# Kernel optimization log

Measured on AMD Instinct MI355X. Metric: run time of the kernel, lower is better.

## Reference

```python
import jax, jax.numpy as jnp
import numpy as np

N_NODES = 50000
N_EDGES = 800000
IN_C, HID_C, OUT_C = 128, 128, 40


def gcn_conv(x, W, b, src, dst, dinv):
    # x: [N, Fin] -> [N, Fout]; PyG GCNConv: h = W x, then sym-normalized
    # aggregation over edges (incl. self-loops), plus bias.
    h = x @ W  # [N, Fout]
    norm = dinv[src] * dinv[dst]  # [E+N]
    msg = h[src] * norm[:, None]  # gather + scale, [E+N, Fout]
    out = jax.ops.segment_sum(msg, dst, num_segments=x.shape[0])
    return out + b


def _prep_edges(edge_index, n):
    # add self-loops; compute deg^{-1/2} with unit edge weights
    loop = jnp.arange(n, dtype=edge_index.dtype)
    src = jnp.concatenate([edge_index[0], loop])
    dst = jnp.concatenate([edge_index[1], loop])
    deg = jax.ops.segment_sum(jnp.ones_like(dst, dtype=jnp.float32), dst, num_segments=n)
    dinv = jnp.where(deg > 0, jax.lax.rsqrt(jnp.maximum(deg, 1.0)), 0.0)
    return src, dst, dinv


def setup_inputs() -> dict:
    key = jax.random.key(0)
    ks = jax.random.split(key, 5)
    x = jax.random.normal(ks[0], (N_NODES, IN_C), dtype=jnp.float32)
    edge_index = jax.random.randint(ks[1], (2, N_EDGES), 0, N_NODES, dtype=jnp.int32)
    s = 0.05
    W1 = jax.random.normal(ks[2], (IN_C, HID_C), dtype=jnp.float32) * s
    W2 = jax.random.normal(ks[3], (HID_C, HID_C), dtype=jnp.float32) * s
    W3 = jax.random.normal(ks[4], (HID_C, OUT_C), dtype=jnp.float32) * s
    return {
        "x": x, "edge_index": edge_index,
        "W1": W1, "b1": jnp.zeros((HID_C,), jnp.float32),
        "W2": W2, "b2": jnp.zeros((HID_C,), jnp.float32),
        "W3": W3, "b3": jnp.zeros((OUT_C,), jnp.float32),
    }


def reference(x, edge_index, W1, b1, W2, b2, W3, b3):
    n = x.shape[0]
    src, dst, dinv = _prep_edges(edge_index, n)
    h = jax.nn.relu(gcn_conv(x, W1, b1, src, dst, dinv))  # dropout = id (eval)
    h = jax.nn.relu(gcn_conv(h, W2, b2, src, dst, dinv))
    h = gcn_conv(h, W3, b3, src, dst, dinv)
    return jax.nn.log_softmax(h, axis=1)
```

## Files before the change

kernel.cpp:

```cpp
#include <hip/hip_runtime.h>
#include <cmath>

__device__ __forceinline__ unsigned short f2bf(float f) {
  unsigned u = __float_as_uint(f);
  u = (u + 0x7FFFu + ((u >> 16) & 1u)) >> 16;
  return (unsigned short)u;
}
__device__ __forceinline__ unsigned pack2(float a, float b) {
  return (unsigned)f2bf(a) | ((unsigned)f2bf(b) << 16);
}
__device__ __forceinline__ float bflo(unsigned u) { return __uint_as_float(u << 16); }
__device__ __forceinline__ float bfhi(unsigned u) { return __uint_as_float(u & 0xFFFF0000u); }
__device__ __forceinline__ float bf1(unsigned short h) { return __uint_as_float((unsigned)h << 16); }

__device__ __forceinline__ unsigned char fp8e(float v) {
  unsigned u = __float_as_uint(v * 0x1.0p-120f);
  unsigned s = (u >> 24) & 0x80u;
  u &= 0x7FFFFFFFu;
  u = u + 0x000FFFFFu + ((u >> 20) & 1u);
  return (unsigned char)(s | ((u >> 20) & 0x7Fu));
}
__device__ __forceinline__ float fp8d(unsigned b) {
  unsigned u = ((b & 0x80u) << 24) | ((b & 0x7Fu) << 20);
  return __uint_as_float(u) * 0x1.0p120f;
}

using bh8 = __attribute__((ext_vector_type(8))) short;
using f32x4 = __attribute__((ext_vector_type(4))) float;

#define BK_STRIDE 8192

__global__ __launch_bounds__(256) void k_bin(const int* __restrict__ src, const int* __restrict__ dst,
                                             int* __restrict__ bucketCur, unsigned* __restrict__ bucketBuf,
                                             int E, int chunk, const float* __restrict__ x,
                                             unsigned short* __restrict__ xb, int total4) {
  __shared__ int hist[256], base[256], cur[256];
  int t = threadIdx.x;
  hist[t] = 0;
  cur[t] = 0;
  __syncthreads();
  int s0 = blockIdx.x * chunk;
  int s1 = min(E, s0 + chunk);
  for (int i = s0 + t; i < s1; i += 256) atomicAdd(&hist[dst[i] >> 8], 1);
  __syncthreads();
  if (hist[t] > 0) base[t] = atomicAdd(&bucketCur[t], hist[t]);
  __syncthreads();
  for (int i = s0 + t; i < s1; i += 256) {
    int d = dst[i];
    int b = d >> 8;
    int r = base[b] + atomicAdd(&cur[b], 1);
    if (r < BK_STRIDE)
      bucketBuf[(size_t)b * BK_STRIDE + r] = (unsigned)src[i] | ((unsigned)(d & 255) << 16);
  }
  int tid = blockIdx.x * 256 + t;
  int stride = gridDim.x * 256;
  for (int i = tid; i < total4; i += stride) {
    float4 v = *(const float4*)&x[(size_t)i * 4];
    uint2 o;
    o.x = pack2(v.x, v.y);
    o.y = pack2(v.z, v.w);
    *(uint2*)&xb[(size_t)i * 4] = o;
  }
}

__global__ __launch_bounds__(256) void k_scan_wt(const int* __restrict__ bucketCur, int* __restrict__ bucketBase,
                                                 int* __restrict__ rp, int nbk, int n, int E,
                                                 const float* __restrict__ W1, const float* __restrict__ W2,
                                                 const float* __restrict__ W3, unsigned short* __restrict__ Wt1,
                                                 unsigned short* __restrict__ Wt2, unsigned short* __restrict__ Wt3) {
  int t = threadIdx.x;
  if (blockIdx.x == 0) {
    __shared__ int s[256];
    int v = (t < nbk) ? bucketCur[t] : 0;
    s[t] = v;
    __syncthreads();
    for (int off = 1; off < 256; off <<= 1) {
      int u = (t >= off) ? s[t - off] : 0;
      __syncthreads();
      s[t] += u;
      __syncthreads();
    }
    if (t < nbk) bucketBase[t] = s[t] - v;
    if (t == 0) rp[n] = E;
    return;
  }
  int i = (blockIdx.x - 1) * 256 + t;
  if (i < 16384) {
    int c = i >> 7, k = i & 127;
    Wt1[i] = f2bf(W1[(size_t)k * 128 + c]);
  } else if (i < 32768) {
    int j = i - 16384;
    int c = j >> 7, k = j & 127;
    Wt2[j] = f2bf(W2[(size_t)k * 128 + c]);
  } else if (i < 32768 + 6144) {
    int j = i - 32768;
    int c = j >> 7, k = j & 127;
    Wt3[j] = (c < 40) ? f2bf(W3[(size_t)k * 40 + c]) : (unsigned short)0;
  }
}

__global__ __launch_bounds__(256) void k_build(const unsigned* __restrict__ bucketBuf,
                                               const int* __restrict__ bucketCnt,
                                               const int* __restrict__ bucketBase, int* __restrict__ rp,
                                               float* __restrict__ dinv, int* __restrict__ csr, int n) {
  __shared__ int hist[256], excl[256], cur[256], s[256];
  int b = blockIdx.x, t = threadIdx.x;
  int cntE = bucketCnt[b];
  int e0 = bucketBase[b];
  const unsigned* buf = bucketBuf + (size_t)b * BK_STRIDE;
  hist[t] = 0;
  cur[t] = 0;
  __syncthreads();
  for (int i = t; i < cntE; i += 256) atomicAdd(&hist[(buf[i] >> 16) & 255], 1);
  __syncthreads();
  int h = hist[t];
  s[t] = h;
  __syncthreads();
  for (int off = 1; off < 256; off <<= 1) {
    int u = (t >= off) ? s[t - off] : 0;
    __syncthreads();
    s[t] += u;
    __syncthreads();
  }
  excl[t] = s[t] - h;
  int node = (b << 8) + t;
  if (node < n) {
    rp[node] = e0 + excl[t];
    dinv[node] = rsqrtf((float)(h + 1));
  }
  __syncthreads();
  for (int i = t; i < cntE; i += 256) {
    unsigned p = buf[i];
    int lo = (p >> 16) & 255;
    int r = atomicAdd(&cur[lo], 1);
    csr[e0 + excl[lo] + r] = (int)(p & 0xFFFFu);
  }
}

template <int WT_N, int NW_COL, int MOUT, bool OUT8>
__global__ __launch_bounds__(256) void k_mfma_gemm(const unsigned short* __restrict__ A,
                                                   const unsigned short* __restrict__ Bt,
                                                   const float* __restrict__ dinv,
                                                   void* __restrict__ Gv, int n) {
  constexpr int NW_ROW = 4 / NW_COL;
  int tid = threadIdx.x;
  int wid = tid >> 6, lane = tid & 63;
  int lr = lane & 15, lq = lane >> 4;
  int wrow = wid / NW_COL, wcol = wid % NW_COL;
  int rowBase = blockIdx.x * (NW_ROW * 32) + wrow * 32;
  int colBase = wcol * (WT_N * 16);

  bh8 af[2][4];
#pragma unroll
  for (int rt = 0; rt < 2; rt++) {
    int row = rowBase + rt * 16 + lr;
    const unsigned short* ap = A + (size_t)row * 128 + lq * 8;
    bool ok = row < n;
#pragma unroll
    for (int ks = 0; ks < 4; ks++) {
      bh8 z = {0, 0, 0, 0, 0, 0, 0, 0};
      af[rt][ks] = ok ? *(const bh8*)(ap + ks * 32) : z;
    }
  }
  bh8 bfr[WT_N][4];
#pragma unroll
  for (int ct = 0; ct < WT_N; ct++) {
    const unsigned short* bp = Bt + (size_t)(colBase + ct * 16 + lr) * 128 + lq * 8;
#pragma unroll
    for (int ks = 0; ks < 4; ks++) bfr[ct][ks] = *(const bh8*)(bp + ks * 32);
  }

  f32x4 acc[2][WT_N];
#pragma unroll
  for (int rt = 0; rt < 2; rt++)
#pragma unroll
    for (int ct = 0; ct < WT_N; ct++) acc[rt][ct] = (f32x4){0.f, 0.f, 0.f, 0.f};

#pragma unroll
  for (int ks = 0; ks < 4; ks++)
#pragma unroll
    for (int rt = 0; rt < 2; rt++)
#pragma unroll
      for (int ct = 0; ct < WT_N; ct++)
        acc[rt][ct] = __builtin_amdgcn_mfma_f32_16x16x32_bf16(af[rt][ks], bfr[ct][ks], acc[rt][ct], 0, 0, 0);

#pragma unroll
  for (int rt = 0; rt < 2; rt++)
#pragma unroll
    for (int r = 0; r < 4; r++) {
      int row = rowBase + rt * 16 + lq * 4 + r;
      if (row < n) {
        float di = dinv[row];
#pragma unroll
        for (int ct = 0; ct < WT_N; ct++) {
          int col = colBase + ct * 16 + lr;
          if (MOUT == 128 || col < MOUT) {
            if constexpr (OUT8)
              ((unsigned char*)Gv)[(size_t)row * MOUT + col] = fp8e(acc[rt][ct][r] * di);
            else
              ((unsigned short*)Gv)[(size_t)row * MOUT + col] = f2bf(acc[rt][ct][r] * di);
          }
        }
      }
    }
}

__global__ __launch_bounds__(256) void k_agg_relu128_f8(const unsigned char* __restrict__ g8,
                                                        const int* __restrict__ csr, const int* __restrict__ rp,
                                                        const float* __restrict__ dinv, const float* __restrict__ bias,
                                                        unsigned short* __restrict__ out, int n) {
  int t = threadIdx.x;
  int node = blockIdx.x * 8 + (t >> 5);
  if (node >= n) return;
  int c = t & 31;
  const unsigned* g32 = (const unsigned*)g8;
  int e0 = rp[node], e1 = rp[node + 1];

  float4 a[8];
  {
    unsigned v = g32[(size_t)node * 32 + c];
    a[0] = make_float4(fp8d(v & 0xFF), fp8d((v >> 8) & 0xFF), fp8d((v >> 16) & 0xFF), fp8d(v >> 24));
  }
#pragma unroll
  for (int u = 1; u < 8; u++) a[u] = make_float4(0.f, 0.f, 0.f, 0.f);

  int e = e0;
  for (; e + 8 <= e1; e += 8) {
    int s[8];
#pragma unroll
    for (int u = 0; u < 8; u++) s[u] = csr[e + u];
    unsigned v[8];
#pragma unroll
    for (int u = 0; u < 8; u++) v[u] = g32[(size_t)s[u] * 32 + c];
#pragma unroll
    for (int u = 0; u < 8; u++) {
      a[u].x += fp8d(v[u] & 0xFF);
      a[u].y += fp8d((v[u] >> 8) & 0xFF);
      a[u].z += fp8d((v[u] >> 16) & 0xFF);
      a[u].w += fp8d(v[u] >> 24);
    }
  }
  for (; e < e1; ++e) {
    unsigned v = g32[(size_t)csr[e] * 32 + c];
    a[0].x += fp8d(v & 0xFF);
    a[0].y += fp8d((v >> 8) & 0xFF);
    a[0].z += fp8d((v >> 16) & 0xFF);
    a[0].w += fp8d(v >> 24);
  }
#pragma unroll
  for (int u = 4; u < 8; u++) {
    a[u - 4].x += a[u].x; a[u - 4].y += a[u].y; a[u - 4].z += a[u].z; a[u - 4].w += a[u].w;
  }
#pragma unroll
  for (int u = 2; u < 4; u++) {
    a[u - 2].x += a[u].x; a[u - 2].y += a[u].y; a[u - 2].z += a[u].z; a[u - 2].w += a[u].w;
  }
  float4 acc = make_float4(a[0].x + a[1].x, a[0].y + a[1].y, a[0].z + a[1].z, a[0].w + a[1].w);

  float di = dinv[node];
  float4 bb = *(const float4*)&bias[c * 4];
  uint2 o;
  o.x = pack2(fmaxf(fmaf(di, acc.x, bb.x), 0.f), fmaxf(fmaf(di, acc.y, bb.y), 0.f));
  o.y = pack2(fmaxf(fmaf(di, acc.z, bb.z), 0.f), fmaxf(fmaf(di, acc.w, bb.w), 0.f));
  *(uint2*)&out[(size_t)node * 128 + c * 4] = o;
}

__global__ __launch_bounds__(256) void k_agg_lsm40(const unsigned short* __restrict__ g,
                                                   const int* __restrict__ csr, const int* __restrict__ rp,
                                                   const float* __restrict__ dinv, const float* __restrict__ bias,
                                                   float* __restrict__ out, int n) {
  int lane = threadIdx.x & 63;
  int node = blockIdx.x * 4 + (threadIdx.x >> 6);
  if (node >= n) return;
  int e0 = rp[node], e1 = rp[node + 1];

  float a[8];
  a[0] = bf1(g[(size_t)node * 40 + lane]);
#pragma unroll
  for (int u = 1; u < 8; u++) a[u] = 0.f;

  int e = e0;
  for (; e + 8 <= e1; e += 8) {
    int s[8];
#pragma unroll
    for (int u = 0; u < 8; u++) s[u] = csr[e + u];
#pragma unroll
    for (int u = 0; u < 8; u++) a[u] += bf1(g[(size_t)s[u] * 40 + lane]);
  }
  for (; e < e1; ++e) a[0] += bf1(g[(size_t)csr[e] * 40 + lane]);

  float acc = ((a[0] + a[1]) + (a[2] + a[3])) + ((a[4] + a[5]) + (a[6] + a[7]));

  bool act = lane < 40;
  float v = act ? fmaf(dinv[node], acc, bias[lane]) : -INFINITY;
  float m = v;
#pragma unroll
  for (int off = 32; off > 0; off >>= 1) m = fmaxf(m, __shfl_xor(m, off, 64));
  float ex = act ? __expf(v - m) : 0.f;
  float ssum = ex;
#pragma unroll
  for (int off = 32; off > 0; off >>= 1) ssum += __shfl_xor(ssum, off, 64);
  if (act) out[(size_t)node * 40 + lane] = v - m - __logf(ssum);
}


extern "C" void kernel_launch(void* const* d_in, const int* in_sizes, int n_in,
                              void* d_out, int out_size, void* d_ws, size_t ws_size,
                              hipStream_t stream) {
  const float* x  = (const float*)d_in[0];
  const int*   ei = (const int*)d_in[1];
  const float* W1 = (const float*)d_in[2];
  const float* b1 = (const float*)d_in[3];
  const float* W2 = (const float*)d_in[4];
  const float* b2 = (const float*)d_in[5];
  const float* W3 = (const float*)d_in[6];
  const float* b3 = (const float*)d_in[7];
  float* out = (float*)d_out;
  int n = in_sizes[0] / 128;
  int E = in_sizes[1] / 2;
  const int* esrc = ei;
  const int* edst = ei + E;
  int nbk = (n + 255) >> 8;

  size_t off = 0;
  auto alloc = [&](size_t bytes) -> void* {
    void* r = (char*)d_ws + off;
    off += (bytes + 255) & ~(size_t)255;
    return r;
  };
  int*      bucketCur  = (int*)alloc(256 * 4);
  int*      bucketBase = (int*)alloc(257 * 4);
  unsigned* bucketBuf  = (unsigned*)alloc((size_t)nbk * BK_STRIDE * 4);
  int*      rp         = (int*)alloc((size_t)(n + 1) * 4);
  float*    dinv       = (float*)alloc((size_t)n * 4);
  int*      csr        = (int*)alloc((size_t)E * 4);
  unsigned short* xb   = (unsigned short*)alloc((size_t)n * 128 * 2 + 4096);
  unsigned short* bufB = (unsigned short*)alloc((size_t)n * 128 * 2 + 4096);
  unsigned char*  gq   = (unsigned char*)alloc((size_t)n * 128 + 4096);
  unsigned short* Wt1  = (unsigned short*)alloc(128 * 128 * 2);
  unsigned short* Wt2  = (unsigned short*)alloc(128 * 128 * 2);
  unsigned short* Wt3  = (unsigned short*)alloc(48 * 128 * 2);

  hipMemsetAsync(bucketCur, 0, 256 * 4, stream);

  const int BIN_BLOCKS = 512;
  int chunk = (E + BIN_BLOCKS - 1) / BIN_BLOCKS;
  int t4 = n * 128 / 4;
  k_bin<<<BIN_BLOCKS, 256, 0, stream>>>(esrc, edst, bucketCur, bucketBuf, E, chunk, x, xb, t4);
  k_scan_wt<<<1 + 152, 256, 0, stream>>>(bucketCur, bucketBase, rp, nbk, n, E, W1, W2, W3, Wt1, Wt2, Wt3);
  k_build<<<nbk, 256, 0, stream>>>(bucketBuf, bucketCur, bucketBase, rp, dinv, csr, n);

  k_mfma_gemm<4, 2, 128, true><<<(n + 63) / 64, 256, 0, stream>>>(xb, Wt1, dinv, gq, n);
  k_agg_relu128_f8<<<(n + 7) / 8, 256, 0, stream>>>(gq, csr, rp, dinv, b1, bufB, n);
  k_mfma_gemm<4, 2, 128, true><<<(n + 63) / 64, 256, 0, stream>>>(bufB, Wt2, dinv, gq, n);
  k_agg_relu128_f8<<<(n + 7) / 8, 256, 0, stream>>>(gq, csr, rp, dinv, b2, xb, n);
  unsigned short* g3 = (unsigned short*)gq;
  k_mfma_gemm<3, 1, 40, false><<<(n + 127) / 128, 256, 0, stream>>>(xb, Wt3, dinv, g3, n);
  k_agg_lsm40<<<(n + 3) / 4, 256, 0, stream>>>(g3, csr, rp, dinv, b3, out, n);
}
```

Measured before the change: 202.1 us.

## Fuse x conversion into GEMM, merge scan into build, use fp8 for layer 3

Removes the separate fp32-to-bf16 pass over x: the first GEMM now reads fp32 x directly and packs it to bf16 in registers. The bucket prefix scan moves into k_build, where each block recomputes it redundantly, and the weight transposes move into k_bin, which drops one kernel launch. The last layer's GEMM output is now stored as fp8 instead of bf16, halving gather traffic in the final aggregation at the cost of extra precision loss before log-softmax.

```diff
diff --git a/kernel.cpp b/kernel.cpp
--- a/kernel.cpp
+++ b/kernel.cpp
@@ -32,8 +32,10 @@
 
 __global__ __launch_bounds__(256) void k_bin(const int* __restrict__ src, const int* __restrict__ dst,
                                              int* __restrict__ bucketCur, unsigned* __restrict__ bucketBuf,
-                                             int E, int chunk, const float* __restrict__ x,
-                                             unsigned short* __restrict__ xb, int total4) {
+                                             int E, int chunk,
+                                             const float* __restrict__ W1, const float* __restrict__ W2,
+                                             const float* __restrict__ W3, unsigned short* __restrict__ Wt1,
+                                             unsigned short* __restrict__ Wt2, unsigned short* __restrict__ Wt3) {
   __shared__ int hist[256], base[256], cur[256];
   int t = threadIdx.x;
   hist[t] = 0;
@@ -54,67 +56,30 @@
   }
   int tid = blockIdx.x * 256 + t;
   int stride = gridDim.x * 256;
-  for (int i = tid; i < total4; i += stride) {
-    float4 v = *(const float4*)&x[(size_t)i * 4];
-    uint2 o;
-    o.x = pack2(v.x, v.y);
-    o.y = pack2(v.z, v.w);
-    *(uint2*)&xb[(size_t)i * 4] = o;
-  }
-}
-
-__global__ __launch_bounds__(256) void k_scan_wt(const int* __restrict__ bucketCur, int* __restrict__ bucketBase,
-                                                 int* __restrict__ rp, int nbk, int n, int E,
-                                                 const float* __restrict__ W1, const float* __restrict__ W2,
-                                                 const float* __restrict__ W3, unsigned short* __restrict__ Wt1,
-                                                 unsigned short* __restrict__ Wt2, unsigned short* __restrict__ Wt3) {
-  int t = threadIdx.x;
-  if (blockIdx.x == 0) {
-    __shared__ int s[256];
-    int v = (t < nbk) ? bucketCur[t] : 0;
-    s[t] = v;
-    __syncthreads();
-    for (int off = 1; off < 256; off <<= 1) {
-      int u = (t >= off) ? s[t - off] : 0;
-      __syncthreads();
-      s[t] += u;
-      __syncthreads();
+  for (int i = tid; i < 32768 + 6144; i += stride) {
+    if (i < 16384) {
+      int c = i >> 7, k = i & 127;
+      Wt1[i] = f2bf(W1[(size_t)k * 128 + c]);
+    } else if (i < 32768) {
+      int j = i - 16384;
+      int c = j >> 7, k = j & 127;
+      Wt2[j] = f2bf(W2[(size_t)k * 128 + c]);
+    } else {
+      int j = i - 32768;
+      int c = j >> 7, k = j & 127;
+      Wt3[j] = (c < 40) ? f2bf(W3[(size_t)k * 40 + c]) : (unsigned short)0;
     }
-    if (t < nbk) bucketBase[t] = s[t] - v;
-    if (t == 0) rp[n] = E;
-    return;
-  }
-  int i = (blockIdx.x - 1) * 256 + t;
-  if (i < 16384) {
-    int c = i >> 7, k = i & 127;
-    Wt1[i] = f2bf(W1[(size_t)k * 128 + c]);
-  } else if (i < 32768) {
-    int j = i - 16384;
-    int c = j >> 7, k = j & 127;
-    Wt2[j] = f2bf(W2[(size_t)k * 128 + c]);
-  } else if (i < 32768 + 6144) {
-    int j = i - 32768;
-    int c = j >> 7, k = j & 127;
-    Wt3[j] = (c < 40) ? f2bf(W3[(size_t)k * 40 + c]) : (unsigned short)0;
   }
 }
 
 __global__ __launch_bounds__(256) void k_build(const unsigned* __restrict__ bucketBuf,
-                                               const int* __restrict__ bucketCnt,
-                                               const int* __restrict__ bucketBase, int* __restrict__ rp,
-                                               float* __restrict__ dinv, int* __restrict__ csr, int n) {
-  __shared__ int hist[256], excl[256], cur[256], s[256];
+                                               const int* __restrict__ bucketCnt, int* __restrict__ rp,
+                                               float* __restrict__ dinv, int* __restrict__ csr, int n, int nbk) {
+  __shared__ int hist[256], excl[256], cur[256], s[256], bc[256];
   int b = blockIdx.x, t = threadIdx.x;
-  int cntE = bucketCnt[b];
-  int e0 = bucketBase[b];
-  const unsigned* buf = bucketBuf + (size_t)b * BK_STRIDE;
-  hist[t] = 0;
-  cur[t] = 0;
-  __syncthreads();
-  for (int i = t; i < cntE; i += 256) atomicAdd(&hist[(buf[i] >> 16) & 255], 1);
-  __syncthreads();
-  int h = hist[t];
-  s[t] = h;
+  int bv = (t < nbk) ? bucketCnt[t] : 0;
+  bc[t] = bv;
+  s[t] = bv;
   __syncthreads();
   for (int off = 1; off < 256; off <<= 1) {
     int u = (t >= off) ? s[t - off] : 0;
@@ -122,12 +87,32 @@
     s[t] += u;
     __syncthreads();
   }
+  int e0 = s[b] - bc[b];
+  int cntE = bc[b];
+  int Etot = s[nbk - 1];
+  __syncthreads();
+  const unsigned* buf = bucketBuf + (size_t)b * BK_STRIDE;
+  hist[t] = 0;
+  cur[t] = 0;
+  __syncthreads();
+  for (int i = t; i < cntE; i += 256) atomicAdd(&hist[(buf[i] >> 16) & 255], 1);
+  __syncthreads();
+  int h = hist[t];
+  s[t] = h;
+  __syncthreads();
+  for (int off = 1; off < 256; off <<= 1) {
+    int u = (t >= off) ? s[t - off] : 0;
+    __syncthreads();
+    s[t] += u;
+    __syncthreads();
+  }
   excl[t] = s[t] - h;
   int node = (b << 8) + t;
   if (node < n) {
     rp[node] = e0 + excl[t];
     dinv[node] = rsqrtf((float)(h + 1));
   }
+  if (b == nbk - 1 && t == 0) rp[n] = Etot;
   __syncthreads();
   for (int i = t; i < cntE; i += 256) {
     unsigned p = buf[i];
@@ -137,8 +122,8 @@
   }
 }
 
-template <int WT_N, int NW_COL, int MOUT, bool OUT8>
-__global__ __launch_bounds__(256) void k_mfma_gemm(const unsigned short* __restrict__ A,
+template <int WT_N, int NW_COL, int MOUT, bool OUT8, bool A32>
+__global__ __launch_bounds__(256) void k_mfma_gemm(const void* __restrict__ Av,
                                                    const unsigned short* __restrict__ Bt,
                                                    const float* __restrict__ dinv,
                                                    void* __restrict__ Gv, int n) {
@@ -154,12 +139,28 @@
 #pragma unroll
   for (int rt = 0; rt < 2; rt++) {
     int row = rowBase + rt * 16 + lr;
-    const unsigned short* ap = A + (size_t)row * 128 + lq * 8;
     bool ok = row < n;
-#pragma unroll
-    for (int ks = 0; ks < 4; ks++) {
-      bh8 z = {0, 0, 0, 0, 0, 0, 0, 0};
-      af[rt][ks] = ok ? *(const bh8*)(ap + ks * 32) : z;
+    if constexpr (A32) {
+      const float* ap = (const float*)Av + (size_t)row * 128 + lq * 8;
+#pragma unroll
+      for (int ks = 0; ks < 4; ks++) {
+        union { uint4 u; bh8 h; } w;
+        if (ok) {
+          float4 v0 = *(const float4*)(ap + ks * 32);
+          float4 v1 = *(const float4*)(ap + ks * 32 + 4);
+          w.u = make_uint4(pack2(v0.x, v0.y), pack2(v0.z, v0.w), pack2(v1.x, v1.y), pack2(v1.z, v1.w));
+        } else {
+          w.u = make_uint4(0u, 0u, 0u, 0u);
+        }
+        af[rt][ks] = w.h;
+      }
+    } else {
+      const unsigned short* ap = (const unsigned short*)Av + (size_t)row * 128 + lq * 8;
+#pragma unroll
+      for (int ks = 0; ks < 4; ks++) {
+        bh8 z = {0, 0, 0, 0, 0, 0, 0, 0};
+        af[rt][ks] = ok ? *(const bh8*)(ap + ks * 32) : z;
+      }
     }
   }
   bh8 bfr[WT_N][4];
@@ -265,17 +266,17 @@
   *(uint2*)&out[(size_t)node * 128 + c * 4] = o;
 }
 
-__global__ __launch_bounds__(256) void k_agg_lsm40(const unsigned short* __restrict__ g,
-                                                   const int* __restrict__ csr, const int* __restrict__ rp,
-                                                   const float* __restrict__ dinv, const float* __restrict__ bias,
-                                                   float* __restrict__ out, int n) {
+__global__ __launch_bounds__(256) void k_agg_lsm40_f8(const unsigned char* __restrict__ g8,
+                                                      const int* __restrict__ csr, const int* __restrict__ rp,
+                                                      const float* __restrict__ dinv, const float* __restrict__ bias,
+                                                      float* __restrict__ out, int n) {
   int lane = threadIdx.x & 63;
   int node = blockIdx.x * 4 + (threadIdx.x >> 6);
   if (node >= n) return;
   int e0 = rp[node], e1 = rp[node + 1];
 
   float a[8];
-  a[0] = bf1(g[(size_t)node * 40 + lane]);
+  a[0] = fp8d(g8[(size_t)node * 40 + lane]);
 #pragma unroll
   for (int u = 1; u < 8; u++) a[u] = 0.f;
 
@@ -285,9 +286,9 @@
 #pragma unroll
     for (int u = 0; u < 8; u++) s[u] = csr[e + u];
 #pragma unroll
-    for (int u = 0; u < 8; u++) a[u] += bf1(g[(size_t)s[u] * 40 + lane]);
-  }
-  for (; e < e1; ++e) a[0] += bf1(g[(size_t)csr[e] * 40 + lane]);
+    for (int u = 0; u < 8; u++) a[u] += fp8d(g8[(size_t)s[u] * 40 + lane]);
+  }
+  for (; e < e1; ++e) a[0] += fp8d(g8[(size_t)csr[e] * 40 + lane]);
 
   float acc = ((a[0] + a[1]) + (a[2] + a[3])) + ((a[4] + a[5]) + (a[6] + a[7]));
 
@@ -329,13 +330,12 @@
     return r;
   };
   int*      bucketCur  = (int*)alloc(256 * 4);
-  int*      bucketBase = (int*)alloc(257 * 4);
   unsigned* bucketBuf  = (unsigned*)alloc((size_t)nbk * BK_STRIDE * 4);
   int*      rp         = (int*)alloc((size_t)(n + 1) * 4);
   float*    dinv       = (float*)alloc((size_t)n * 4);
   int*      csr        = (int*)alloc((size_t)E * 4);
-  unsigned short* xb   = (unsigned short*)alloc((size_t)n * 128 * 2 + 4096);
   unsigned short* bufB = (unsigned short*)alloc((size_t)n * 128 * 2 + 4096);
+  unsigned short* bufC = (unsigned short*)alloc((size_t)n * 128 * 2 + 4096);
   unsigned char*  gq   = (unsigned char*)alloc((size_t)n * 128 + 4096);
   unsigned short* Wt1  = (unsigned short*)alloc(128 * 128 * 2);
   unsigned short* Wt2  = (unsigned short*)alloc(128 * 128 * 2);
@@ -345,16 +345,13 @@
 
   const int BIN_BLOCKS = 512;
   int chunk = (E + BIN_BLOCKS - 1) / BIN_BLOCKS;
-  int t4 = n * 128 / 4;
-  k_bin<<<BIN_BLOCKS, 256, 0, stream>>>(esrc, edst, bucketCur, bucketBuf, E, chunk, x, xb, t4);
-  k_scan_wt<<<1 + 152, 256, 0, stream>>>(bucketCur, bucketBase, rp, nbk, n, E, W1, W2, W3, Wt1, Wt2, Wt3);
-  k_build<<<nbk, 256, 0, stream>>>(bucketBuf, bucketCur, bucketBase, rp, dinv, csr, n);
-
-  k_mfma_gemm<4, 2, 128, true><<<(n + 63) / 64, 256, 0, stream>>>(xb, Wt1, dinv, gq, n);
+  k_bin<<<BIN_BLOCKS, 256, 0, stream>>>(esrc, edst, bucketCur, bucketBuf, E, chunk, W1, W2, W3, Wt1, Wt2, Wt3);
+  k_build<<<nbk, 256, 0, stream>>>(bucketBuf, bucketCur, rp, dinv, csr, n, nbk);
+
+  k_mfma_gemm<4, 2, 128, true, true><<<(n + 63) / 64, 256, 0, stream>>>(x, Wt1, dinv, gq, n);
   k_agg_relu128_f8<<<(n + 7) / 8, 256, 0, stream>>>(gq, csr, rp, dinv, b1, bufB, n);
-  k_mfma_gemm<4, 2, 128, true><<<(n + 63) / 64, 256, 0, stream>>>(bufB, Wt2, dinv, gq, n);
-  k_agg_relu128_f8<<<(n + 7) / 8, 256, 0, stream>>>(gq, csr, rp, dinv, b2, xb, n);
-  unsigned short* g3 = (unsigned short*)gq;
-  k_mfma_gemm<3, 1, 40, false><<<(n + 127) / 128, 256, 0, stream>>>(xb, Wt3, dinv, g3, n);
-  k_agg_lsm40<<<(n + 3) / 4, 256, 0, stream>>>(g3, csr, rp, dinv, b3, out, n);
-}
+  k_mfma_gemm<4, 2, 128, true, false><<<(n + 63) / 64, 256, 0, stream>>>(bufB, Wt2, dinv, gq, n);
+  k_agg_relu128_f8<<<(n + 7) / 8, 256, 0, stream>>>(gq, csr, rp, dinv, b2, bufC, n);
+  k_mfma_gemm<3, 1, 40, true, false><<<(n + 127) / 128, 256, 0, stream>>>(bufC, Wt3, dinv, gq, n);
+  k_agg_lsm40_f8<<<(n + 3) / 4, 256, 0, stream>>>(gq, csr, rp, dinv, b3, out, n);
+}
```

Result: faster. 196.8 us (-2.7%).
